# Optimization experiments

Measured on AMD Instinct MI355X. Metric: run time of the kernel, lower is better.

The kernel has to match this reference:

```python
import jax, jax.numpy as jnp
import numpy as np

N, LT, LV, D, H = 4, 1024, 1024, 1024, 16
HD = D // H
EPS = 1e-12


def layernorm(x, w, b):
    u = x.mean(-1, keepdims=True)
    s = ((x - u) ** 2).mean(-1, keepdims=True)
    return w * (x - u) / jnp.sqrt(s + EPS) + b


def attention(q_in, k_in, v_in, mask, qw, qb, kw, kb, vw, vb):
    # mask: (N, Lq_or_1, Lk) float in {0,1}; torch Linear is x @ W.T + b
    def heads(x, w, b):
        y = x @ w.T + b
        return y.reshape(y.shape[0], y.shape[1], H, HD).transpose(0, 2, 1, 3)  # (N,H,L,hd)
    q, k, v = heads(q_in, qw, qb), heads(k_in, kw, kb), heads(v_in, vw, vb)
    scores = jnp.einsum('bhqd,bhkd->bhqk', q, k) / np.sqrt(HD).astype(np.float32)
    scores = scores + (1.0 - mask[:, None]) * (-10000.0)
    probs = jax.nn.softmax(scores, axis=-1)  # dropout is identity in eval
    ctx = jnp.einsum('bhqk,bhkd->bhqd', probs, v)
    return ctx.transpose(0, 2, 1, 3).reshape(q_in.shape[0], q_in.shape[1], D)


def setup_inputs() -> dict:
    key = jax.random.key(0)
    ks = jax.random.split(key, 16)
    inp = {
        'dec_hidden_states': jax.random.normal(ks[0], (N, LT, D), jnp.float32),
        'enc_outputs': jax.random.normal(ks[1], (N, LV, D), jnp.float32),
        'dec_mask': jnp.ones((N, LT), jnp.float32),
        'enc_mask': jnp.ones((N, LV), jnp.float32),
    }
    wnames = ['sa_qw', 'sa_kw', 'sa_vw', 'ca_qw', 'ca_kw', 'ca_vw', 'out_w']
    for i, n in enumerate(wnames):
        inp[n] = jax.random.normal(ks[2 + i], (D, D), jnp.float32) * 0.02
    for n in ['sa_qb', 'sa_kb', 'sa_vb', 'ca_qb', 'ca_kb', 'ca_vb', 'out_b', 'n1_b', 'n2_b', 'out_ln_b']:
        inp[n] = jnp.zeros((D,), jnp.float32)
    for n in ['n1_w', 'n2_w', 'out_ln_w']:
        inp[n] = jnp.ones((D,), jnp.float32)
    return inp


def reference(dec_hidden_states, enc_outputs, dec_mask, enc_mask,
              sa_qw, sa_qb, sa_kw, sa_kb, sa_vw, sa_vb, n1_w, n1_b,
              ca_qw, ca_qb, ca_kw, ca_kb, ca_vw, ca_vb, n2_w, n2_b,
              out_w, out_b, out_ln_w, out_ln_b):
    Lt = dec_mask.shape[1]
    # diagonal_mask=True: causal tril combined with padding mask
    self_mask = dec_mask[:, None, :] * jnp.tril(jnp.ones((Lt, Lt), dec_mask.dtype))  # (N,Lt,Lt)
    a = attention(dec_hidden_states, dec_hidden_states, dec_hidden_states, self_mask,
                  sa_qw, sa_qb, sa_kw, sa_kb, sa_vw, sa_vb)
    a = layernorm(a + dec_hidden_states, n1_w, n1_b)
    c = attention(a, enc_outputs, enc_outputs, enc_mask[:, None, :],
                  ca_qw, ca_qb, ca_kw, ca_kb, ca_vw, ca_vb)
    c = layernorm(a + c, n2_w, n2_b)
    # BertOutput called as output(x, x): dense, residual, LN (dropout = identity)
    h = c @ out_w.T + out_b
    return layernorm(h + c, out_ln_w, out_ln_b)
```

## Files before the change

kernel.cpp:

```cpp
#include <hip/hip_runtime.h>
#include <cstdint>
#include <cstddef>

typedef __bf16 bf16x8 __attribute__((ext_vector_type(8)));
typedef float  floatx4 __attribute__((ext_vector_type(4)));
typedef unsigned short ushortx8 __attribute__((ext_vector_type(8)));
typedef unsigned short ushortx4 __attribute__((ext_vector_type(4)));

#define MFMA16(a, b, c) __builtin_amdgcn_mfma_f32_16x16x32_bf16((a), (b), (c), 0, 0, 0)

__device__ inline unsigned short f2bf(float f) {
    unsigned int u = __float_as_uint(f);
    unsigned int r = (u + 0x7fffu + ((u >> 16) & 1u)) >> 16;
    return (unsigned short)r;
}

struct Src2 { const float* p[2]; };
__global__ __launch_bounds__(256) void k_x2_to_bf16(Src2 s2, unsigned short* __restrict__ dst) {
    int i = blockIdx.x * 256 + threadIdx.x;
    const float* src = s2.p[i >> 19];
    int off = i & 524287;
    const float4* s = (const float4*)src + (size_t)off * 2;
    float4 x0 = s[0], x1 = s[1];
    ushortx8 o;
    o[0] = f2bf(x0.x); o[1] = f2bf(x0.y); o[2] = f2bf(x0.z); o[3] = f2bf(x0.w);
    o[4] = f2bf(x1.x); o[5] = f2bf(x1.y); o[6] = f2bf(x1.z); o[7] = f2bf(x1.w);
    *((ushortx8*)dst + i) = o;
}
struct Src7 { const float* p[7]; };
__global__ __launch_bounds__(256) void k_w7_to_bf16(Src7 s7, unsigned short* __restrict__ dst) {
    int i = blockIdx.x * 256 + threadIdx.x;
    const float* src = s7.p[i >> 17];
    int off = i & 131071;
    const float4* s = (const float4*)src + (size_t)off * 2;
    float4 x0 = s[0], x1 = s[1];
    ushortx8 o;
    o[0] = f2bf(x0.x); o[1] = f2bf(x0.y); o[2] = f2bf(x0.z); o[3] = f2bf(x0.w);
    o[4] = f2bf(x1.x); o[5] = f2bf(x1.y); o[6] = f2bf(x1.z); o[7] = f2bf(x1.w);
    *((ushortx8*)dst + i) = o;
}

template <int MODE>
__global__ __launch_bounds__(256) void k_gemm_bias(const unsigned short* __restrict__ A,
                                                   const unsigned short* __restrict__ A2,
                                                   const unsigned short* __restrict__ W,
                                                   const float* __restrict__ bias0,
                                                   const float* __restrict__ bias1,
                                                   const float* __restrict__ bias2,
                                                   void* __restrict__ d0,
                                                   void* __restrict__ d1,
                                                   void* __restrict__ d2,
                                                   int K) {
    __shared__ __align__(16) unsigned short As[128 * 64];
    __shared__ __align__(16) unsigned short Bs[128 * 64];
    const int tid = threadIdx.x;
    const int wave = tid >> 6, lane = tid & 63;
    const int quad = lane >> 4, l15 = lane & 15;
    const int wm = wave >> 1, wn = wave & 1;

    constexpr int NT = (MODE == 3) ? 8 : 24;
    int fid = blockIdx.y * 32 + blockIdx.x;
    int xcd = fid & 7, idx = fid >> 3;
    const int m0 = (xcd * 4 + idx / NT) * 128;
    const int n0 = (idx % NT) * 128;
    const int sect_blk = n0 >> 10;

    const unsigned short* Ause = (MODE == 4 && sect_blk != 0) ? A2 : A;

    const size_t rowbytes = (size_t)K * 2;
    const int idx0 = tid, idx1 = 256 + tid;
    const char* pA0 = (const char*)Ause + (size_t)(m0 + (idx0 >> 2)) * rowbytes + ((idx0 & 3) << 4);
    const char* pA1 = (const char*)Ause + (size_t)(m0 + (idx1 >> 2)) * rowbytes + ((idx1 & 3) << 4);
    const char* pB0 = (const char*)W + (size_t)(n0 + (idx0 >> 2)) * rowbytes + ((idx0 & 3) << 4);
    const char* pB1 = (const char*)W + (size_t)(n0 + (idx1 >> 2)) * rowbytes + ((idx1 & 3) << 4);

    int4 a0a = *(const int4*)pA0, a0b = *(const int4*)(pA0 + 64);
    int4 a1a = *(const int4*)pA1, a1b = *(const int4*)(pA1 + 64);
    int4 b0a = *(const int4*)pB0, b0b = *(const int4*)(pB0 + 64);
    int4 b1a = *(const int4*)pB1, b1b = *(const int4*)(pB1 + 64);

    floatx4 acc[4][4] = {};

    const int KT = K >> 6;
    for (int kt = 0; kt < KT; ++kt) {
        __syncthreads();
        ((int4*)As)[idx0] = a0a; ((int4*)As)[idx1] = a1a;
        ((int4*)As)[512 + idx0] = a0b; ((int4*)As)[512 + idx1] = a1b;
        ((int4*)Bs)[idx0] = b0a; ((int4*)Bs)[idx1] = b1a;
        ((int4*)Bs)[512 + idx0] = b0b; ((int4*)Bs)[512 + idx1] = b1b;
        __syncthreads();
        if (kt + 1 < KT) {
            pA0 += 128; pA1 += 128; pB0 += 128; pB1 += 128;
            a0a = *(const int4*)pA0; a0b = *(const int4*)(pA0 + 64);
            a1a = *(const int4*)pA1; a1b = *(const int4*)(pA1 + 64);
            b0a = *(const int4*)pB0; b0b = *(const int4*)(pB0 + 64);
            b1a = *(const int4*)pB1; b1b = *(const int4*)(pB1 + 64);
        }
        const char* Asb = (const char*)As;
        const char* Bsb = (const char*)Bs;
#pragma unroll
        for (int half = 0; half < 2; ++half) {
            const int hb = half * 8192;
            bf16x8 af[4], bfr[4];
#pragma unroll
            for (int r = 0; r < 4; ++r)
                af[r] = *(const bf16x8*)(Asb + hb + ((wm * 64 + r * 16 + l15) * 64 + quad * 16));
#pragma unroll
            for (int c = 0; c < 4; ++c)
                bfr[c] = *(const bf16x8*)(Bsb + hb + ((wn * 64 + c * 16 + l15) * 64 + quad * 16));
#pragma unroll
            for (int r = 0; r < 4; ++r)
#pragma unroll
                for (int c = 0; c < 4; ++c)
                    acc[r][c] = MFMA16(af[r], bfr[c], acc[r][c]);
        }
    }

#pragma unroll
    for (int c = 0; c < 4; ++c) {
        int col = n0 + wn * 64 + c * 16 + l15;
        int sect = col >> 10, cc = col & 1023;
        float bv;
        if (MODE == 3) bv = bias0[col];
        else bv = (sect == 0 ? bias0 : (sect == 1 ? bias1 : bias2))[cc];
        int h = cc >> 6, d = cc & 63;
#pragma unroll
        for (int r = 0; r < 4; ++r) {
            int mrow = m0 + wm * 64 + r * 16 + quad * 4;
#pragma unroll
            for (int i = 0; i < 4; ++i) {
                float v = acc[r][c][i] + bv;
                int row = mrow + i;
                if (MODE == 3) {
                    ((float*)d0)[(size_t)row * 1024 + col] = v;
                } else {
                    int b = row >> 10, l = row & 1023;
                    unsigned short* base = (unsigned short*)(sect == 0 ? d0 : (sect == 1 ? d1 : d2));
                    bool isV = (sect == 2);
                    size_t off;
                    if (isV) {
                        int kk = l & 31;
                        int kperm = ((kk & 15) << 1) | (kk >> 4);
                        off = (size_t)(b * 16 + h) * 65536 + (size_t)(l >> 5) * 2048 + d * 32 + kperm;
                    } else {
                        off = ((size_t)(b * 16 + h) * 1024 + l) * 64 + d;
                    }
                    base[off] = f2bf(v);
                }
            }
        }
    }
}

__global__ __launch_bounds__(256, 2) void k_flash_attn(const unsigned short* __restrict__ Qp,
                                                       const unsigned short* __restrict__ Kp,
                                                       const unsigned short* __restrict__ Vp,
                                                       const float* __restrict__ mask,
                                                       float* __restrict__ ctx,
                                                       int causal) {
    const int L = 1024, D = 1024;
    const float SC = 0.18033688011112042f;
    int f = blockIdx.x;
    int g = f >> 6;
    int bh = (f & 7) + (g << 3);
    int qt = ((f >> 3) + g) & 7;
    int h = bh & 15, b = bh >> 4;
    int tid = threadIdx.x;
    int wave = tid >> 6, lane = tid & 63, quad = lane >> 4, l15 = lane & 15;
    int qbase = qt * 128 + wave * 32;

    __shared__ __align__(16) unsigned short Ks[4096];
    __shared__ __align__(16) unsigned short Vs[5120];
    __shared__ float penf[1024];
    __shared__ __align__(16) unsigned short Plds[4 * 1280];

    {
        float4 mv = ((const float4*)(mask + b * L))[tid];
        float4 pv;
        pv.x = (1.0f - mv.x) * -14426.950408889634f;
        pv.y = (1.0f - mv.y) * -14426.950408889634f;
        pv.z = (1.0f - mv.z) * -14426.950408889634f;
        pv.w = (1.0f - mv.w) * -14426.950408889634f;
        ((float4*)penf)[tid] = pv;
    }

    const unsigned short* Qh = Qp + ((size_t)(b * 16 + h) * 1024 + qbase) * 64;
    bf16x8 qf[2][2];
#pragma unroll
    for (int qh = 0; qh < 2; ++qh) {
        qf[qh][0] = *(const bf16x8*)(Qh + (qh * 16 + l15) * 64 + quad * 8);
        qf[qh][1] = *(const bf16x8*)(Qh + (qh * 16 + l15) * 64 + 32 + quad * 8);
    }

    const char* Kh = (const char*)(Kp + (size_t)(b * 16 + h) * 65536);
    const char* Vh = (const char*)(Vp + (size_t)(b * 16 + h) * 65536);

    int ktiles = causal ? (2 * qt + 2) : 16;

    char* Ksb = (char*)Ks;
    char* Vsb = (char*)Vs;
    int krow = tid >> 3, kblk = tid & 7;
    int kd0 = krow * 128 + ((kblk ^ (krow & 7)) << 4);
    int kd1 = kd0 + 32 * 128;
    int vd0 = (tid >> 2) * 80 + ((tid & 3) << 4);
    int vd1 = vd0 + 5120;

    int karA[4], karB[4];
#pragma unroll
    for (int r = 0; r < 4; ++r) {
        int row = r * 16 + l15;
        karA[r] = row * 128 + ((quad ^ (l15 & 7)) << 4);
        karB[r] = row * 128 + (((quad | 4) ^ (l15 & 7)) << 4);
    }
    int var_[8];
#pragma unroll
    for (int s = 0; s < 2; ++s)
#pragma unroll
        for (int fi = 0; fi < 4; ++fi)
            var_[s * 4 + fi] = s * 5120 + (fi * 16 + l15) * 80 + (quad << 4);

    floatx4 O[2][4] = {};
    float lsum[2][4] = {};
    unsigned short* pw = &Plds[wave * 1280];
    unsigned int* pw32 = (unsigned int*)pw;

    int4 ka0 = *(const int4*)(Kh + tid * 16);
    int4 ka1 = *(const int4*)(Kh + 4096 + tid * 16);
    int4 va0 = *(const int4*)(Vh + tid * 16);
    int4 va1 = *(const int4*)(Vh + 4096 + tid * 16);

    for (int kt = 0; kt < ktiles; ++kt) {
        *(int4*)(Ksb + kd0) = ka0;
        *(int4*)(Ksb + kd1) = ka1;
        *(int4*)(Vsb + vd0) = va0;
        *(int4*)(Vsb + vd1) = va1;
        __syncthreads();
        if (kt + 1 < ktiles) {
            const char* Kg = Kh + (size_t)(kt + 1) * 8192;
            const char* Vg = Vh + (size_t)(kt + 1) * 8192;
            ka0 = *(const int4*)(Kg + tid * 16);
            ka1 = *(const int4*)(Kg + 4096 + tid * 16);
            va0 = *(const int4*)(Vg + tid * 16);
            va1 = *(const int4*)(Vg + 4096 + tid * 16);
        }
        int k0 = kt * 64;

        if (!(causal && k0 > qbase + 31)) {
            bf16x8 kA[4], kB[4];
#pragma unroll
            for (int r = 0; r < 4; ++r) {
                kA[r] = *(const bf16x8*)(Ksb + karA[r]);
                kB[r] = *(const bf16x8*)(Ksb + karB[r]);
            }
            bf16x8 vv[8];
#pragma unroll
            for (int s = 0; s < 8; ++s) vv[s] = *(const bf16x8*)(Vsb + var_[s]);
            float pr0 = penf[k0 + l15];
            float pr1 = penf[k0 + 16 + l15];
            float pr2 = penf[k0 + 32 + l15];
            float pr3 = penf[k0 + 48 + l15];

#pragma unroll
            for (int qh = 0; qh < 2; ++qh) {
                int qlo = qbase + qh * 16;
                if (causal && k0 > qlo + 15) continue;
                bool boundary = causal && (k0 + 63 > qlo);

                floatx4 S0 = {}, S1 = {}, S2 = {}, S3 = {};
                S0 = MFMA16(qf[qh][0], kA[0], S0); S0 = MFMA16(qf[qh][1], kB[0], S0);
                S1 = MFMA16(qf[qh][0], kA[1], S1); S1 = MFMA16(qf[qh][1], kB[1], S1);
                S2 = MFMA16(qf[qh][0], kA[2], S2); S2 = MFMA16(qf[qh][1], kB[2], S2);
                S3 = MFMA16(qf[qh][0], kA[3], S3); S3 = MFMA16(qf[qh][1], kB[3], S3);

                int qrow = qlo + quad * 4;
#pragma unroll
                for (int i = 0; i < 4; ++i) {
                    float x0 = fmaf(S0[i], SC, pr0);
                    float x1 = fmaf(S1[i], SC, pr1);
                    float x2 = fmaf(S2[i], SC, pr2);
                    float x3 = fmaf(S3[i], SC, pr3);
                    if (boundary) {
                        int q = qrow + i;
                        x0 = ((k0 + l15) <= q) ? x0 : -50000.0f;
                        x1 = ((k0 + 16 + l15) <= q) ? x1 : -50000.0f;
                        x2 = ((k0 + 32 + l15) <= q) ? x2 : -50000.0f;
                        x3 = ((k0 + 48 + l15) <= q) ? x3 : -50000.0f;
                    }
                    float p0 = __builtin_amdgcn_exp2f(x0);
                    float p1 = __builtin_amdgcn_exp2f(x1);
                    float p2 = __builtin_amdgcn_exp2f(x2);
                    float p3 = __builtin_amdgcn_exp2f(x3);
                    lsum[qh][i] += (p0 + p1) + (p2 + p3);
                    unsigned r0 = __float_as_uint(p0) + 0x8000u;
                    unsigned r1 = __float_as_uint(p1) + 0x8000u;
                    unsigned r2 = __float_as_uint(p2) + 0x8000u;
                    unsigned r3 = __float_as_uint(p3) + 0x8000u;
                    unsigned plo = __builtin_amdgcn_perm(r1, r0, 0x07060302u);
                    unsigned phi = __builtin_amdgcn_perm(r3, r2, 0x07060302u);
                    int ro = (quad * 4 + i) * 20;
                    pw32[ro + l15] = plo;
                    pw32[320 + ro + l15] = phi;
                }
                bf16x8 pa_lo = *(const bf16x8*)(pw + l15 * 40 + quad * 8);
                bf16x8 pa_hi = *(const bf16x8*)(pw + 640 + l15 * 40 + quad * 8);
                O[qh][0] = MFMA16(pa_lo, vv[0], O[qh][0]);
                O[qh][1] = MFMA16(pa_lo, vv[1], O[qh][1]);
                O[qh][2] = MFMA16(pa_lo, vv[2], O[qh][2]);
                O[qh][3] = MFMA16(pa_lo, vv[3], O[qh][3]);
                O[qh][0] = MFMA16(pa_hi, vv[4], O[qh][0]);
                O[qh][1] = MFMA16(pa_hi, vv[5], O[qh][1]);
                O[qh][2] = MFMA16(pa_hi, vv[6], O[qh][2]);
                O[qh][3] = MFMA16(pa_hi, vv[7], O[qh][3]);
            }
        }
        __syncthreads();
    }

#pragma unroll
    for (int qh = 0; qh < 2; ++qh)
#pragma unroll
        for (int i = 0; i < 4; ++i) {
            float l = lsum[qh][i];
            l += __shfl_xor(l, 1);
            l += __shfl_xor(l, 2);
            l += __shfl_xor(l, 4);
            l += __shfl_xor(l, 8);
            float inv = 1.0f / l;
            int q = qbase + qh * 16 + quad * 4 + i;
            float* op = ctx + ((size_t)(b * L + q)) * D + h * 64;
#pragma unroll
            for (int fi = 0; fi < 4; ++fi) op[fi * 16 + l15] = O[qh][fi][i] * inv;
        }
}

__global__ __launch_bounds__(256) void k_add_ln(const float* __restrict__ X,
                                                const float* __restrict__ Y,
                                                const float* __restrict__ w,
                                                const float* __restrict__ bvec,
                                                float* __restrict__ outf,
                                                unsigned short* __restrict__ outbf) {
    int row = blockIdx.x;
    int tid = threadIdx.x;
    float4 x = *((const float4*)(X + (size_t)row * 1024) + tid);
    float4 y = *((const float4*)(Y + (size_t)row * 1024) + tid);
    float v0 = x.x + y.x, v1 = x.y + y.y, v2 = x.z + y.z, v3 = x.w + y.w;
    float s = v0 + v1 + v2 + v3;
    float s2 = v0 * v0 + v1 * v1 + v2 * v2 + v3 * v3;
#pragma unroll
    for (int off = 32; off > 0; off >>= 1) {
        s += __shfl_xor(s, off);
        s2 += __shfl_xor(s2, off);
    }
    __shared__ float red[8];
    int wave = tid >> 6, lane = tid & 63;
    if (lane == 0) { red[wave] = s; red[4 + wave] = s2; }
    __syncthreads();
    s = red[0] + red[1] + red[2] + red[3];
    s2 = red[4] + red[5] + red[6] + red[7];
    float u = s * (1.0f / 1024.0f);
    float var = s2 * (1.0f / 1024.0f) - u * u;
    float r = 1.0f / sqrtf(fmaxf(var, 0.0f) + 1e-12f);
    float4 wv = *((const float4*)w + tid);
    float4 bv = *((const float4*)bvec + tid);
    float o0 = wv.x * (v0 - u) * r + bv.x;
    float o1 = wv.y * (v1 - u) * r + bv.y;
    float o2 = wv.z * (v2 - u) * r + bv.z;
    float o3 = wv.w * (v3 - u) * r + bv.w;
    float4 o = {o0, o1, o2, o3};
    *((float4*)(outf + (size_t)row * 1024) + tid) = o;
    if (outbf) {
        ushortx4 ob;
        ob[0] = f2bf(o0); ob[1] = f2bf(o1); ob[2] = f2bf(o2); ob[3] = f2bf(o3);
        *((ushortx4*)outbf + (size_t)row * 256 + tid) = ob;
    }
}

extern "C" void kernel_launch(void* const* d_in, const int* in_sizes, int n_in,
                              void* d_out, int out_size, void* d_ws, size_t ws_size,
                              hipStream_t stream) {
    (void)in_sizes; (void)n_in; (void)out_size; (void)ws_size;
    const float* dec = (const float*)d_in[0];
    const float* enc = (const float*)d_in[1];
    const float* dec_mask = (const float*)d_in[2];
    const float* enc_mask = (const float*)d_in[3];
    const float* b_saq = (const float*)d_in[11];
    const float* b_sak = (const float*)d_in[12];
    const float* b_sav = (const float*)d_in[13];
    const float* b_caq = (const float*)d_in[14];
    const float* b_cak = (const float*)d_in[15];
    const float* b_cav = (const float*)d_in[16];
    const float* b_out = (const float*)d_in[17];
    const float* n1_b = (const float*)d_in[18];
    const float* n2_b = (const float*)d_in[19];
    const float* oln_b = (const float*)d_in[20];
    const float* n1_w = (const float*)d_in[21];
    const float* n2_w = (const float*)d_in[22];
    const float* oln_w = (const float*)d_in[23];

    char* ws = (char*)d_ws;
    const size_t MB2 = 2097152;
    const size_t ACT_BF = 8388608;
    const size_t ACT_F32 = 16777216;
    unsigned short* Wbf[7];
    for (int i = 0; i < 7; ++i) Wbf[i] = (unsigned short*)(ws + i * MB2);
    size_t off = 7 * MB2;
    unsigned short* Xbf = (unsigned short*)(ws + off); off += ACT_BF;
    unsigned short* Ebf = (unsigned short*)(ws + off); off += ACT_BF;
    unsigned short* Abf = (unsigned short*)(ws + off); off += ACT_BF;
    unsigned short* Cbf = (unsigned short*)(ws + off); off += ACT_BF;
    unsigned short* Qp = (unsigned short*)(ws + off); off += ACT_BF;
    unsigned short* Kp = (unsigned short*)(ws + off); off += ACT_BF;
    unsigned short* Vp = (unsigned short*)(ws + off); off += ACT_BF;
    float* ctx = (float*)(ws + off); off += ACT_F32;
    float* a_f32 = (float*)(ws + off); off += ACT_F32;
    float* c_f32 = (float*)(ws + off); off += ACT_F32;
    float* h_f32 = ctx;
    float* outp = (float*)d_out;

    dim3 blk(256);
    dim3 attn_grid(512);

    Src2 s2; s2.p[0] = dec; s2.p[1] = enc;
    k_x2_to_bf16<<<dim3(4096), blk, 0, stream>>>(s2, Xbf);
    Src7 s7;
    for (int i = 0; i < 7; ++i) s7.p[i] = (const float*)d_in[4 + i];
    k_w7_to_bf16<<<dim3(3584), blk, 0, stream>>>(s7, Wbf[0]);

    k_gemm_bias<0><<<dim3(32, 24), blk, 0, stream>>>(Xbf, Xbf, Wbf[0], b_saq, b_sak, b_sav,
                                                     Qp, Kp, Vp, 1024);
    k_flash_attn<<<attn_grid, blk, 0, stream>>>(Qp, Kp, Vp, dec_mask, ctx, 1);
    k_add_ln<<<dim3(4096), blk, 0, stream>>>(ctx, dec, n1_w, n1_b, a_f32, Abf);

    k_gemm_bias<4><<<dim3(32, 24), blk, 0, stream>>>(Abf, Ebf, Wbf[3], b_caq, b_cak, b_cav,
                                                     Qp, Kp, Vp, 1024);
    k_flash_attn<<<attn_grid, blk, 0, stream>>>(Qp, Kp, Vp, enc_mask, ctx, 0);
    k_add_ln<<<dim3(4096), blk, 0, stream>>>(a_f32, ctx, n2_w, n2_b, c_f32, Cbf);

    k_gemm_bias<3><<<dim3(32, 8), blk, 0, stream>>>(Cbf, Cbf, Wbf[6], b_out, b_out, b_out,
                                                    h_f32, nullptr, nullptr, 1024);
    k_add_ln<<<dim3(4096), blk, 0, stream>>>(h_f32, c_f32, oln_w, oln_b, outp, (unsigned short*)nullptr);
}
```

Measured before the change: 331.1 us.

## Halve attention query tile to 64 rows and double grid size

Each attention block now processes 64 query rows (16 per wave) instead of 128 (32 per wave), so the grid grows from 512 to 1024 blocks and launch bounds allow 4 blocks per CU. This is meant to raise occupancy and improve load balance for the causal triangle, and to cut register pressure by dropping the per-wave second query half. In exchange, each K/V tile staged in LDS is reused by half as many query rows, which roughly doubles K/V global loads and staging work.

New measurement: 338.3 us. 1.02x slower.

```diff
diff --git a/kernel.cpp b/kernel.cpp
--- a/kernel.cpp
+++ b/kernel.cpp
@@ -152,7 +152,7 @@
     }
 }
 
-__global__ __launch_bounds__(256, 2) void k_flash_attn(const unsigned short* __restrict__ Qp,
+__global__ __launch_bounds__(256, 4) void k_flash_attn(const unsigned short* __restrict__ Qp,
                                                        const unsigned short* __restrict__ Kp,
                                                        const unsigned short* __restrict__ Vp,
                                                        const float* __restrict__ mask,
@@ -161,13 +161,13 @@
     const int L = 1024, D = 1024;
     const float SC = 0.18033688011112042f;
     int f = blockIdx.x;
-    int g = f >> 6;
+    int g = f >> 7;
+    int qi = ((f >> 3) + g) & 15;
     int bh = (f & 7) + (g << 3);
-    int qt = ((f >> 3) + g) & 7;
     int h = bh & 15, b = bh >> 4;
     int tid = threadIdx.x;
     int wave = tid >> 6, lane = tid & 63, quad = lane >> 4, l15 = lane & 15;
-    int qbase = qt * 128 + wave * 32;
+    int qbase = qi * 64 + wave * 16;
 
     __shared__ __align__(16) unsigned short Ks[4096];
     __shared__ __align__(16) unsigned short Vs[5120];
@@ -185,17 +185,13 @@
     }
 
     const unsigned short* Qh = Qp + ((size_t)(b * 16 + h) * 1024 + qbase) * 64;
-    bf16x8 qf[2][2];
-#pragma unroll
-    for (int qh = 0; qh < 2; ++qh) {
-        qf[qh][0] = *(const bf16x8*)(Qh + (qh * 16 + l15) * 64 + quad * 8);
-        qf[qh][1] = *(const bf16x8*)(Qh + (qh * 16 + l15) * 64 + 32 + quad * 8);
-    }
+    bf16x8 qf0 = *(const bf16x8*)(Qh + l15 * 64 + quad * 8);
+    bf16x8 qf1 = *(const bf16x8*)(Qh + l15 * 64 + 32 + quad * 8);
 
     const char* Kh = (const char*)(Kp + (size_t)(b * 16 + h) * 65536);
     const char* Vh = (const char*)(Vp + (size_t)(b * 16 + h) * 65536);
 
-    int ktiles = causal ? (2 * qt + 2) : 16;
+    int ktiles = causal ? (qi + 1) : 16;
 
     char* Ksb = (char*)Ks;
     char* Vsb = (char*)Vs;
@@ -219,8 +215,8 @@
         for (int fi = 0; fi < 4; ++fi)
             var_[s * 4 + fi] = s * 5120 + (fi * 16 + l15) * 80 + (quad << 4);
 
-    floatx4 O[2][4] = {};
-    float lsum[2][4] = {};
+    floatx4 O[4] = {};
+    float lsum[4] = {};
     unsigned short* pw = &Plds[wave * 1280];
     unsigned int* pw32 = (unsigned int*)pw;
 
@@ -245,7 +241,9 @@
         }
         int k0 = kt * 64;
 
-        if (!(causal && k0 > qbase + 31)) {
+        if (!(causal && k0 > qbase + 15)) {
+            bool boundary = causal && (k0 + 63 > qbase);
+
             bf16x8 kA[4], kB[4];
 #pragma unroll
             for (int r = 0; r < 4; ++r) {
@@ -260,77 +258,68 @@
             float pr2 = penf[k0 + 32 + l15];
             float pr3 = penf[k0 + 48 + l15];
 
-#pragma unroll
-            for (int qh = 0; qh < 2; ++qh) {
-                int qlo = qbase + qh * 16;
-                if (causal && k0 > qlo + 15) continue;
-                bool boundary = causal && (k0 + 63 > qlo);
-
-                floatx4 S0 = {}, S1 = {}, S2 = {}, S3 = {};
-                S0 = MFMA16(qf[qh][0], kA[0], S0); S0 = MFMA16(qf[qh][1], kB[0], S0);
-                S1 = MFMA16(qf[qh][0], kA[1], S1); S1 = MFMA16(qf[qh][1], kB[1], S1);
-                S2 = MFMA16(qf[qh][0], kA[2], S2); S2 = MFMA16(qf[qh][1], kB[2], S2);
-                S3 = MFMA16(qf[qh][0], kA[3], S3); S3 = MFMA16(qf[qh][1], kB[3], S3);
-
-                int qrow = qlo + quad * 4;
-#pragma unroll
-                for (int i = 0; i < 4; ++i) {
-                    float x0 = fmaf(S0[i], SC, pr0);
-                    float x1 = fmaf(S1[i], SC, pr1);
-                    float x2 = fmaf(S2[i], SC, pr2);
-                    float x3 = fmaf(S3[i], SC, pr3);
-                    if (boundary) {
-                        int q = qrow + i;
-                        x0 = ((k0 + l15) <= q) ? x0 : -50000.0f;
-                        x1 = ((k0 + 16 + l15) <= q) ? x1 : -50000.0f;
-                        x2 = ((k0 + 32 + l15) <= q) ? x2 : -50000.0f;
-                        x3 = ((k0 + 48 + l15) <= q) ? x3 : -50000.0f;
-                    }
-                    float p0 = __builtin_amdgcn_exp2f(x0);
-                    float p1 = __builtin_amdgcn_exp2f(x1);
-                    float p2 = __builtin_amdgcn_exp2f(x2);
-                    float p3 = __builtin_amdgcn_exp2f(x3);
-                    lsum[qh][i] += (p0 + p1) + (p2 + p3);
-                    unsigned r0 = __float_as_uint(p0) + 0x8000u;
-                    unsigned r1 = __float_as_uint(p1) + 0x8000u;
-                    unsigned r2 = __float_as_uint(p2) + 0x8000u;
-                    unsigned r3 = __float_as_uint(p3) + 0x8000u;
-                    unsigned plo = __builtin_amdgcn_perm(r1, r0, 0x07060302u);
-                    unsigned phi = __builtin_amdgcn_perm(r3, r2, 0x07060302u);
-                    int ro = (quad * 4 + i) * 20;
-                    pw32[ro + l15] = plo;
-                    pw32[320 + ro + l15] = phi;
+            floatx4 S0 = {}, S1 = {}, S2 = {}, S3 = {};
+            S0 = MFMA16(qf0, kA[0], S0); S0 = MFMA16(qf1, kB[0], S0);
+            S1 = MFMA16(qf0, kA[1], S1); S1 = MFMA16(qf1, kB[1], S1);
+            S2 = MFMA16(qf0, kA[2], S2); S2 = MFMA16(qf1, kB[2], S2);
+            S3 = MFMA16(qf0, kA[3], S3); S3 = MFMA16(qf1, kB[3], S3);
+
+            int qrow = qbase + quad * 4;
+#pragma unroll
+            for (int i = 0; i < 4; ++i) {
+                float x0 = fmaf(S0[i], SC, pr0);
+                float x1 = fmaf(S1[i], SC, pr1);
+                float x2 = fmaf(S2[i], SC, pr2);
+                float x3 = fmaf(S3[i], SC, pr3);
+                if (boundary) {
+                    int q = qrow + i;
+                    x0 = ((k0 + l15) <= q) ? x0 : -50000.0f;
+                    x1 = ((k0 + 16 + l15) <= q) ? x1 : -50000.0f;
+                    x2 = ((k0 + 32 + l15) <= q) ? x2 : -50000.0f;
+                    x3 = ((k0 + 48 + l15) <= q) ? x3 : -50000.0f;
                 }
-                bf16x8 pa_lo = *(const bf16x8*)(pw + l15 * 40 + quad * 8);
-                bf16x8 pa_hi = *(const bf16x8*)(pw + 640 + l15 * 40 + quad * 8);
-                O[qh][0] = MFMA16(pa_lo, vv[0], O[qh][0]);
-                O[qh][1] = MFMA16(pa_lo, vv[1], O[qh][1]);
-                O[qh][2] = MFMA16(pa_lo, vv[2], O[qh][2]);
-                O[qh][3] = MFMA16(pa_lo, vv[3], O[qh][3]);
-                O[qh][0] = MFMA16(pa_hi, vv[4], O[qh][0]);
-                O[qh][1] = MFMA16(pa_hi, vv[5], O[qh][1]);
-                O[qh][2] = MFMA16(pa_hi, vv[6], O[qh][2]);
-                O[qh][3] = MFMA16(pa_hi, vv[7], O[qh][3]);
+                float p0 = __builtin_amdgcn_exp2f(x0);
+                float p1 = __builtin_amdgcn_exp2f(x1);
+                float p2 = __builtin_amdgcn_exp2f(x2);
+                float p3 = __builtin_amdgcn_exp2f(x3);
+                lsum[i] += (p0 + p1) + (p2 + p3);
+                unsigned r0 = __float_as_uint(p0) + 0x8000u;
+                unsigned r1 = __float_as_uint(p1) + 0x8000u;
+                unsigned r2 = __float_as_uint(p2) + 0x8000u;
+                unsigned r3 = __float_as_uint(p3) + 0x8000u;
+                unsigned plo = __builtin_amdgcn_perm(r1, r0, 0x07060302u);
+                unsigned phi = __builtin_amdgcn_perm(r3, r2, 0x07060302u);
+                int ro = (quad * 4 + i) * 20;
+                pw32[ro + l15] = plo;
+                pw32[320 + ro + l15] = phi;
             }
+            bf16x8 pa_lo = *(const bf16x8*)(pw + l15 * 40 + quad * 8);
+            bf16x8 pa_hi = *(const bf16x8*)(pw + 640 + l15 * 40 + quad * 8);
+            O[0] = MFMA16(pa_lo, vv[0], O[0]);
+            O[1] = MFMA16(pa_lo, vv[1], O[1]);
+            O[2] = MFMA16(pa_lo, vv[2], O[2]);
+            O[3] = MFMA16(pa_lo, vv[3], O[3]);
+            O[0] = MFMA16(pa_hi, vv[4], O[0]);
+            O[1] = MFMA16(pa_hi, vv[5], O[1]);
+            O[2] = MFMA16(pa_hi, vv[6], O[2]);
+            O[3] = MFMA16(pa_hi, vv[7], O[3]);
         }
         __syncthreads();
     }
 
 #pragma unroll
-    for (int qh = 0; qh < 2; ++qh)
-#pragma unroll
-        for (int i = 0; i < 4; ++i) {
-            float l = lsum[qh][i];
-            l += __shfl_xor(l, 1);
-            l += __shfl_xor(l, 2);
-            l += __shfl_xor(l, 4);
-            l += __shfl_xor(l, 8);
-            float inv = 1.0f / l;
-            int q = qbase + qh * 16 + quad * 4 + i;
-            float* op = ctx + ((size_t)(b * L + q)) * D + h * 64;
-#pragma unroll
-            for (int fi = 0; fi < 4; ++fi) op[fi * 16 + l15] = O[qh][fi][i] * inv;
-        }
+    for (int i = 0; i < 4; ++i) {
+        float l = lsum[i];
+        l += __shfl_xor(l, 1);
+        l += __shfl_xor(l, 2);
+        l += __shfl_xor(l, 4);
+        l += __shfl_xor(l, 8);
+        float inv = 1.0f / l;
+        int q = qbase + quad * 4 + i;
+        float* op = ctx + ((size_t)(b * L + q)) * D + h * 64;
+#pragma unroll
+        for (int fi = 0; fi < 4; ++fi) op[fi * 16 + l15] = O[fi][i] * inv;
+    }
 }
 
 __global__ __launch_bounds__(256) void k_add_ln(const float* __restrict__ X,
@@ -418,7 +407,7 @@
     float* outp = (float*)d_out;
 
     dim3 blk(256);
-    dim3 attn_grid(512);
+    dim3 attn_grid(1024);
 
     Src2 s2; s2.p[0] = dec; s2.p[1] = enc;
     k_x2_to_bf16<<<dim3(4096), blk, 0, stream>>>(s2, Xbf);
```

## Restructure flash attention with strided query tiles, double-buffered K/V, halved grid

Applied to the files above, without the earlier changes.

Each block now handles four interleaved 64-row query groups (qg + 4j) of one head, so K/V tiles loaded into shared memory are reused by four times as many queries and causal work is balanced across blocks. K/V shared buffers are double-buffered, which removes the trailing barrier per tile, and the next tile's global loads overlap with compute. The grid shrinks from 512 to 256 blocks. In exchange each thread holds more accumulator registers and uses more LDS, which may cut occupancy, and with 256 blocks there may be too few to fill all compute units.

Measured after the change: 351.9 us. 1.06x slower.

```diff
diff --git a/kernel.cpp b/kernel.cpp
--- a/kernel.cpp
+++ b/kernel.cpp
@@ -161,18 +161,16 @@
     const int L = 1024, D = 1024;
     const float SC = 0.18033688011112042f;
     int f = blockIdx.x;
-    int g = f >> 6;
-    int bh = (f & 7) + (g << 3);
-    int qt = ((f >> 3) + g) & 7;
+    int bh = ((f & 7) << 3) | ((f >> 3) & 7);
+    int qg = f >> 6;
     int h = bh & 15, b = bh >> 4;
     int tid = threadIdx.x;
     int wave = tid >> 6, lane = tid & 63, quad = lane >> 4, l15 = lane & 15;
-    int qbase = qt * 128 + wave * 32;
-
-    __shared__ __align__(16) unsigned short Ks[4096];
-    __shared__ __align__(16) unsigned short Vs[5120];
+
+    __shared__ __align__(16) unsigned short Ks[2][4096];
+    __shared__ __align__(16) unsigned short Vs[2][5120];
     __shared__ float penf[1024];
-    __shared__ __align__(16) unsigned short Plds[4 * 1280];
+    __shared__ __align__(16) unsigned short Plds[4][4][1280];
 
     {
         float4 mv = ((const float4*)(mask + b * L))[tid];
@@ -184,21 +182,23 @@
         ((float4*)penf)[tid] = pv;
     }
 
-    const unsigned short* Qh = Qp + ((size_t)(b * 16 + h) * 1024 + qbase) * 64;
-    bf16x8 qf[2][2];
-#pragma unroll
-    for (int qh = 0; qh < 2; ++qh) {
-        qf[qh][0] = *(const bf16x8*)(Qh + (qh * 16 + l15) * 64 + quad * 8);
-        qf[qh][1] = *(const bf16x8*)(Qh + (qh * 16 + l15) * 64 + 32 + quad * 8);
+    int qb[4];
+#pragma unroll
+    for (int j = 0; j < 4; ++j) qb[j] = (qg + 4 * j) * 64 + wave * 16;
+
+    const unsigned short* Qh = Qp + (size_t)(b * 16 + h) * 65536;
+    bf16x8 qf[4][2];
+#pragma unroll
+    for (int j = 0; j < 4; ++j) {
+        qf[j][0] = *(const bf16x8*)(Qh + (qb[j] + l15) * 64 + quad * 8);
+        qf[j][1] = *(const bf16x8*)(Qh + (qb[j] + l15) * 64 + 32 + quad * 8);
     }
 
     const char* Kh = (const char*)(Kp + (size_t)(b * 16 + h) * 65536);
     const char* Vh = (const char*)(Vp + (size_t)(b * 16 + h) * 65536);
 
-    int ktiles = causal ? (2 * qt + 2) : 16;
-
-    char* Ksb = (char*)Ks;
-    char* Vsb = (char*)Vs;
+    int ktiles = causal ? (qg + 13) : 16;
+
     int krow = tid >> 3, kblk = tid & 7;
     int kd0 = krow * 128 + ((kblk ^ (krow & 7)) << 4);
     int kd1 = kd0 + 32 * 128;
@@ -212,30 +212,38 @@
         karA[r] = row * 128 + ((quad ^ (l15 & 7)) << 4);
         karB[r] = row * 128 + (((quad | 4) ^ (l15 & 7)) << 4);
     }
-    int var_[8];
-#pragma unroll
-    for (int s = 0; s < 2; ++s)
-#pragma unroll
-        for (int fi = 0; fi < 4; ++fi)
-            var_[s * 4 + fi] = s * 5120 + (fi * 16 + l15) * 80 + (quad << 4);
-
-    floatx4 O[2][4] = {};
-    float lsum[2][4] = {};
-    unsigned short* pw = &Plds[wave * 1280];
-    unsigned int* pw32 = (unsigned int*)pw;
-
-    int4 ka0 = *(const int4*)(Kh + tid * 16);
-    int4 ka1 = *(const int4*)(Kh + 4096 + tid * 16);
-    int4 va0 = *(const int4*)(Vh + tid * 16);
-    int4 va1 = *(const int4*)(Vh + 4096 + tid * 16);
-
-    for (int kt = 0; kt < ktiles; ++kt) {
+    int varlo[4], varhi[4];
+#pragma unroll
+    for (int fi = 0; fi < 4; ++fi) {
+        varlo[fi] = (fi * 16 + l15) * 80 + (quad << 4);
+        varhi[fi] = varlo[fi] + 5120;
+    }
+
+    floatx4 O[4][4] = {};
+    float lsum[4][4] = {};
+
+    {
+        int4 ka0 = *(const int4*)(Kh + tid * 16);
+        int4 ka1 = *(const int4*)(Kh + 4096 + tid * 16);
+        int4 va0 = *(const int4*)(Vh + tid * 16);
+        int4 va1 = *(const int4*)(Vh + 4096 + tid * 16);
+        char* Ksb = (char*)Ks[0];
+        char* Vsb = (char*)Vs[0];
         *(int4*)(Ksb + kd0) = ka0;
         *(int4*)(Ksb + kd1) = ka1;
         *(int4*)(Vsb + vd0) = va0;
         *(int4*)(Vsb + vd1) = va1;
+    }
+
+    for (int kt = 0; kt < ktiles; ++kt) {
         __syncthreads();
-        if (kt + 1 < ktiles) {
+        int k0 = kt * 64;
+        const char* Ksb = (const char*)Ks[kt & 1];
+        const char* Vsb = (const char*)Vs[kt & 1];
+
+        int4 ka0, ka1, va0, va1;
+        bool more = (kt + 1 < ktiles);
+        if (more) {
             const char* Kg = Kh + (size_t)(kt + 1) * 8192;
             const char* Vg = Vh + (size_t)(kt + 1) * 8192;
             ka0 = *(const int4*)(Kg + tid * 16);
@@ -243,93 +251,107 @@
             va0 = *(const int4*)(Vg + tid * 16);
             va1 = *(const int4*)(Vg + 4096 + tid * 16);
         }
-        int k0 = kt * 64;
-
-        if (!(causal && k0 > qbase + 31)) {
-            bf16x8 kA[4], kB[4];
-#pragma unroll
-            for (int r = 0; r < 4; ++r) {
-                kA[r] = *(const bf16x8*)(Ksb + karA[r]);
-                kB[r] = *(const bf16x8*)(Ksb + karB[r]);
+
+        float pr0 = penf[k0 + l15];
+        float pr1 = penf[k0 + 16 + l15];
+        float pr2 = penf[k0 + 32 + l15];
+        float pr3 = penf[k0 + 48 + l15];
+
+        bf16x8 paL[4], paH[4];
+        bool act[4];
+#pragma unroll
+        for (int j = 0; j < 4; ++j) {
+            act[j] = !(causal && k0 > qb[j] + 15);
+            if (!act[j]) continue;
+            bool boundary = causal && (k0 + 63 > qb[j]);
+
+            floatx4 S0 = {}, S1 = {}, S2 = {}, S3 = {};
+            {
+                bf16x8 kA0 = *(const bf16x8*)(Ksb + karA[0]);
+                bf16x8 kB0 = *(const bf16x8*)(Ksb + karB[0]);
+                S0 = MFMA16(qf[j][0], kA0, S0); S0 = MFMA16(qf[j][1], kB0, S0);
+                bf16x8 kA1 = *(const bf16x8*)(Ksb + karA[1]);
+                bf16x8 kB1 = *(const bf16x8*)(Ksb + karB[1]);
+                S1 = MFMA16(qf[j][0], kA1, S1); S1 = MFMA16(qf[j][1], kB1, S1);
+                bf16x8 kA2 = *(const bf16x8*)(Ksb + karA[2]);
+                bf16x8 kB2 = *(const bf16x8*)(Ksb + karB[2]);
+                S2 = MFMA16(qf[j][0], kA2, S2); S2 = MFMA16(qf[j][1], kB2, S2);
+                bf16x8 kA3 = *(const bf16x8*)(Ksb + karA[3]);
+                bf16x8 kB3 = *(const bf16x8*)(Ksb + karB[3]);
+                S3 = MFMA16(qf[j][0], kA3, S3); S3 = MFMA16(qf[j][1], kB3, S3);
             }
-            bf16x8 vv[8];
-#pragma unroll
-            for (int s = 0; s < 8; ++s) vv[s] = *(const bf16x8*)(Vsb + var_[s]);
-            float pr0 = penf[k0 + l15];
-            float pr1 = penf[k0 + 16 + l15];
-            float pr2 = penf[k0 + 32 + l15];
-            float pr3 = penf[k0 + 48 + l15];
-
-#pragma unroll
-            for (int qh = 0; qh < 2; ++qh) {
-                int qlo = qbase + qh * 16;
-                if (causal && k0 > qlo + 15) continue;
-                bool boundary = causal && (k0 + 63 > qlo);
-
-                floatx4 S0 = {}, S1 = {}, S2 = {}, S3 = {};
-                S0 = MFMA16(qf[qh][0], kA[0], S0); S0 = MFMA16(qf[qh][1], kB[0], S0);
-                S1 = MFMA16(qf[qh][0], kA[1], S1); S1 = MFMA16(qf[qh][1], kB[1], S1);
-                S2 = MFMA16(qf[qh][0], kA[2], S2); S2 = MFMA16(qf[qh][1], kB[2], S2);
-                S3 = MFMA16(qf[qh][0], kA[3], S3); S3 = MFMA16(qf[qh][1], kB[3], S3);
-
-                int qrow = qlo + quad * 4;
-#pragma unroll
-                for (int i = 0; i < 4; ++i) {
-                    float x0 = fmaf(S0[i], SC, pr0);
-                    float x1 = fmaf(S1[i], SC, pr1);
-                    float x2 = fmaf(S2[i], SC, pr2);
-                    float x3 = fmaf(S3[i], SC, pr3);
-                    if (boundary) {
-                        int q = qrow + i;
-                        x0 = ((k0 + l15) <= q) ? x0 : -50000.0f;
-                        x1 = ((k0 + 16 + l15) <= q) ? x1 : -50000.0f;
-                        x2 = ((k0 + 32 + l15) <= q) ? x2 : -50000.0f;
-                        x3 = ((k0 + 48 + l15) <= q) ? x3 : -50000.0f;
-                    }
-                    float p0 = __builtin_amdgcn_exp2f(x0);
-                    float p1 = __builtin_amdgcn_exp2f(x1);
-                    float p2 = __builtin_amdgcn_exp2f(x2);
-                    float p3 = __builtin_amdgcn_exp2f(x3);
-                    lsum[qh][i] += (p0 + p1) + (p2 + p3);
-                    unsigned r0 = __float_as_uint(p0) + 0x8000u;
-                    unsigned r1 = __float_as_uint(p1) + 0x8000u;
-                    unsigned r2 = __float_as_uint(p2) + 0x8000u;
-                    unsigned r3 = __float_as_uint(p3) + 0x8000u;
-                    unsigned plo = __builtin_amdgcn_perm(r1, r0, 0x07060302u);
-                    unsigned phi = __builtin_amdgcn_perm(r3, r2, 0x07060302u);
-                    int ro = (quad * 4 + i) * 20;
-                    pw32[ro + l15] = plo;
-                    pw32[320 + ro + l15] = phi;
+
+            unsigned short* pw = &Plds[wave][j][0];
+            unsigned int* pw32 = (unsigned int*)pw;
+            int qrow = qb[j] + quad * 4;
+#pragma unroll
+            for (int i = 0; i < 4; ++i) {
+                float x0 = fmaf(S0[i], SC, pr0);
+                float x1 = fmaf(S1[i], SC, pr1);
+                float x2 = fmaf(S2[i], SC, pr2);
+                float x3 = fmaf(S3[i], SC, pr3);
+                if (boundary) {
+                    int q = qrow + i;
+                    x0 = ((k0 + l15) <= q) ? x0 : -50000.0f;
+                    x1 = ((k0 + 16 + l15) <= q) ? x1 : -50000.0f;
+                    x2 = ((k0 + 32 + l15) <= q) ? x2 : -50000.0f;
+                    x3 = ((k0 + 48 + l15) <= q) ? x3 : -50000.0f;
                 }
-                bf16x8 pa_lo = *(const bf16x8*)(pw + l15 * 40 + quad * 8);
-                bf16x8 pa_hi = *(const bf16x8*)(pw + 640 + l15 * 40 + quad * 8);
-                O[qh][0] = MFMA16(pa_lo, vv[0], O[qh][0]);
-                O[qh][1] = MFMA16(pa_lo, vv[1], O[qh][1]);
-                O[qh][2] = MFMA16(pa_lo, vv[2], O[qh][2]);
-                O[qh][3] = MFMA16(pa_lo, vv[3], O[qh][3]);
-                O[qh][0] = MFMA16(pa_hi, vv[4], O[qh][0]);
-                O[qh][1] = MFMA16(pa_hi, vv[5], O[qh][1]);
-                O[qh][2] = MFMA16(pa_hi, vv[6], O[qh][2]);
-                O[qh][3] = MFMA16(pa_hi, vv[7], O[qh][3]);
+                float p0 = __builtin_amdgcn_exp2f(x0);
+                float p1 = __builtin_amdgcn_exp2f(x1);
+                float p2 = __builtin_amdgcn_exp2f(x2);
+                float p3 = __builtin_amdgcn_exp2f(x3);
+                lsum[j][i] += (p0 + p1) + (p2 + p3);
+                unsigned r0 = __float_as_uint(p0) + 0x8000u;
+                unsigned r1 = __float_as_uint(p1) + 0x8000u;
+                unsigned r2 = __float_as_uint(p2) + 0x8000u;
+                unsigned r3 = __float_as_uint(p3) + 0x8000u;
+                unsigned plo = __builtin_amdgcn_perm(r1, r0, 0x07060302u);
+                unsigned phi = __builtin_amdgcn_perm(r3, r2, 0x07060302u);
+                int ro = (quad * 4 + i) * 20;
+                pw32[ro + l15] = plo;
+                pw32[320 + ro + l15] = phi;
             }
-        }
-        __syncthreads();
-    }
-
-#pragma unroll
-    for (int qh = 0; qh < 2; ++qh)
+            paL[j] = *(const bf16x8*)(pw + l15 * 40 + quad * 8);
+            paH[j] = *(const bf16x8*)(pw + 640 + l15 * 40 + quad * 8);
+        }
+
+#pragma unroll
+        for (int fi = 0; fi < 4; ++fi) {
+            bf16x8 vlo = *(const bf16x8*)(Vsb + varlo[fi]);
+            bf16x8 vhi = *(const bf16x8*)(Vsb + varhi[fi]);
+#pragma unroll
+            for (int j = 0; j < 4; ++j) {
+                if (!act[j]) continue;
+                O[j][fi] = MFMA16(paL[j], vlo, O[j][fi]);
+                O[j][fi] = MFMA16(paH[j], vhi, O[j][fi]);
+            }
+        }
+
+        if (more) {
+            char* Ksn = (char*)Ks[(kt + 1) & 1];
+            char* Vsn = (char*)Vs[(kt + 1) & 1];
+            *(int4*)(Ksn + kd0) = ka0;
+            *(int4*)(Ksn + kd1) = ka1;
+            *(int4*)(Vsn + vd0) = va0;
+            *(int4*)(Vsn + vd1) = va1;
+        }
+    }
+
+#pragma unroll
+    for (int j = 0; j < 4; ++j)
 #pragma unroll
         for (int i = 0; i < 4; ++i) {
-            float l = lsum[qh][i];
+            float l = lsum[j][i];
             l += __shfl_xor(l, 1);
             l += __shfl_xor(l, 2);
             l += __shfl_xor(l, 4);
             l += __shfl_xor(l, 8);
             float inv = 1.0f / l;
-            int q = qbase + qh * 16 + quad * 4 + i;
+            int q = qb[j] + quad * 4 + i;
             float* op = ctx + ((size_t)(b * L + q)) * D + h * 64;
 #pragma unroll
-            for (int fi = 0; fi < 4; ++fi) op[fi * 16 + l15] = O[qh][fi][i] * inv;
+            for (int fi = 0; fi < 4; ++fi) op[fi * 16 + l15] = O[j][fi][i] * inv;
         }
 }
 
@@ -418,7 +440,7 @@
     float* outp = (float*)d_out;
 
     dim3 blk(256);
-    dim3 attn_grid(512);
+    dim3 attn_grid(256);
 
     Src2 s2; s2.p[0] = dec; s2.p[1] = enc;
     k_x2_to_bf16<<<dim3(4096), blk, 0, stream>>>(s2, Xbf);
```
